# Performance work log

Measured on AMD Instinct MI355X. Metric: run time of the kernel, lower is better.

Reference implementation:

```python
import jax, jax.numpy as jnp
import numpy as np

B, T, DIM, H = 2, 2048, 1024, 16
HD = DIM // H


def setup_inputs() -> dict:
    key = jax.random.key(0)
    k1, k2, k3 = jax.random.split(key, 3)
    std = 1.0 / np.sqrt(DIM)
    x = jax.random.normal(k1, (B, T, DIM), dtype=jnp.float32)
    # torch Linear(dim, 3*dim).weight is [3*dim, dim]; we store the transposed
    # [dim, 3*dim] layout so forward is x @ W_qkv (same math).
    W_qkv = jax.random.uniform(k2, (DIM, 3 * DIM), dtype=jnp.float32, minval=-std, maxval=std)
    W_proj = jax.random.uniform(k3, (DIM, DIM), dtype=jnp.float32, minval=-std, maxval=std)
    return {"x": x, "W_qkv": W_qkv, "W_proj": W_proj}


def reference(x, W_qkv, W_proj):
    Bv, Tv, C = x.shape
    # qkv projection -> [B, T, 3, H, HD] -> q,k,v each [B, H, T, HD]
    qkv = (x @ W_qkv).reshape(Bv, Tv, 3, H, HD)
    qkv = jnp.transpose(qkv, (2, 0, 3, 1, 4))
    q, k, v = qkv[0], qkv[1], qkv[2]
    scale = jnp.asarray(np.sqrt(HD), dtype=x.dtype)
    scores = jnp.einsum('bhqd,bhkd->bhqk', q, k) / scale
    causal = jnp.tril(jnp.ones((Tv, Tv), dtype=bool))  # [T, T]
    scores = jnp.where(causal[None, None, :, :], scores, -jnp.inf)
    attn = jax.nn.softmax(scores, axis=-1)  # [B, H, T, T]
    # entropy per query position, averaged over heads -> [B, T]
    entropy = -(attn * jnp.log(attn + 1e-9)).sum(axis=-1).mean(axis=1)
    # dropout is identity in eval mode
    out = jnp.einsum('bhqk,bhkd->bhqd', attn, v)
    out = jnp.transpose(out, (0, 2, 1, 3)).reshape(Bv, Tv, C)
    return out @ W_proj, entropy
```

## Files before the change

### kernel.cpp

```cpp
#include <hip/hip_runtime.h>


typedef unsigned short u16;
typedef __attribute__((ext_vector_type(8))) __bf16 bf16x8;
typedef __attribute__((ext_vector_type(4))) float float4v;

#define BQ 2
#define TQ 2048
#define DIMQ 1024
#define HQ 16
#define HDQ 64

__device__ __forceinline__ float4v mfma16(bf16x8 a, bf16x8 b, float4v c) {
    return __builtin_amdgcn_mfma_f32_16x16x32_bf16(a, b, c, 0, 0, 0);
}

__device__ __forceinline__ u16 f2bf(float f) {
    unsigned x = __float_as_uint(f);
    return (u16)((x + 0x7FFFu + ((x >> 16) & 1u)) >> 16);
}

__device__ __forceinline__ uint4 cvt8(float4 a, float4 b) {
    union { uint4 v; u16 u[8]; } r;
    r.u[0] = f2bf(a.x); r.u[1] = f2bf(a.y); r.u[2] = f2bf(a.z); r.u[3] = f2bf(a.w);
    r.u[4] = f2bf(b.x); r.u[5] = f2bf(b.y); r.u[6] = f2bf(b.z); r.u[7] = f2bf(b.w);
    return r.v;
}

__device__ __forceinline__ void async16(const u16* g, u16* l) {
    __builtin_amdgcn_global_load_lds(
        (const __attribute__((address_space(1))) void*)g,
        (__attribute__((address_space(3))) void*)l, 16, 0, 0);
}

__device__ __forceinline__ void tr_tile(
    const float* __restrict__ in, u16* __restrict__ out, int R, int C,
    int tx, int ty, int tid, float (*T)[68])
{
    const int k0 = ty * 64, n0 = tx * 64;
    {
        int r = tid >> 2, cc = (tid & 3) << 4;
        const float* src = in + (size_t)(k0 + r) * C + n0 + cc;
        float4 v0 = ((const float4*)src)[0];
        float4 v1 = ((const float4*)src)[1];
        float4 v2 = ((const float4*)src)[2];
        float4 v3 = ((const float4*)src)[3];
        *(float4*)&T[r][cc + 0]  = v0;
        *(float4*)&T[r][cc + 4]  = v1;
        *(float4*)&T[r][cc + 8]  = v2;
        *(float4*)&T[r][cc + 12] = v3;
    }
    __syncthreads();
    {
        int nr = tid >> 2, kc = (tid & 3) << 4;
        union { uint4 v; u16 u[8]; } o0, o1;
#pragma unroll
        for (int j = 0; j < 8; ++j) o0.u[j] = f2bf(T[kc + j][nr]);
#pragma unroll
        for (int j = 0; j < 8; ++j) o1.u[j] = f2bf(T[kc + 8 + j][nr]);
        u16* dst = out + (size_t)(n0 + nr) * R + k0 + kc;
        ((uint4*)dst)[0] = o0.v;
        *(uint4*)(dst + 8) = o1.v;
    }
}

__global__ __launch_bounds__(256) void prep_kernel(
    const float* __restrict__ x, const float* __restrict__ Wq,
    const float* __restrict__ Wp,
    u16* __restrict__ xb, u16* __restrict__ Wt, u16* __restrict__ Wpt)
{
    __shared__ float T[64][68];
    const int bx = blockIdx.x, tid = threadIdx.x;
    if (bx < 2048) {
        int i = (bx * 256 + tid) * 8;
        float4 a = *(const float4*)(x + i);
        float4 b = *(const float4*)(x + i + 4);
        *(uint4*)(xb + i) = cvt8(a, b);
    } else if (bx < 2816) {
        int bb = bx - 2048;
        tr_tile(Wq, Wt, DIMQ, 3 * DIMQ, bb % 48, bb / 48, tid, T);
    } else {
        int bb = bx - 2816;
        tr_tile(Wp, Wpt, DIMQ, DIMQ, bb & 15, bb >> 4, tid, T);
    }
}

__global__ __launch_bounds__(256) void tr_cvt(
    const float* __restrict__ in, u16* __restrict__ out, int R, int C)
{
    __shared__ float T[64][68];
    tr_tile(in, out, R, C, blockIdx.x, blockIdx.y, threadIdx.x, T);
}

template <int TILEM, int MODE>
__global__ __launch_bounds__(256) void gemm_db(
    const u16* __restrict__ A, const u16* __restrict__ Bt,
    int M, int N, int K,
    u16* __restrict__ Qo, u16* __restrict__ Ko, u16* __restrict__ Vt,
    float* __restrict__ Of, const float* __restrict__ EntIn)
{
    constexpr int MT = TILEM / 32;
    constexpr int AR = TILEM / 64;
    __shared__ u16 As[2][TILEM * 32];
    __shared__ u16 Bs[2][128 * 32];

    const int tid = threadIdx.x;
    const int bm = blockIdx.y, bn = blockIdx.x;
    const int wave = tid >> 6, lane = tid & 63;
    const int quad = lane >> 4, c = lane & 15;
    const int wm = wave >> 1, wn = wave & 1;
    const int x3 = c & 3;

    const float4v z = {0.f, 0.f, 0.f, 0.f};
    float4v acc[MT][4];
#pragma unroll
    for (int mt = 0; mt < MT; ++mt)
#pragma unroll
        for (int tn = 0; tn < 4; ++tn) acc[mt][tn] = z;

    const int srow = tid >> 2;
    const int schunk8 = (((tid & 3) ^ (srow & 3)) << 3);
    const u16* ga = A  + (size_t)(bm * TILEM + srow) * K + schunk8;
    const u16* gb = Bt + (size_t)(bn * 128  + srow) * K + schunk8;

#pragma unroll
    for (int p = 0; p < AR; ++p)
        async16(ga + (size_t)(p * 64) * K, As[0] + p * 2048 + tid * 8);
#pragma unroll
    for (int p = 0; p < 2; ++p)
        async16(gb + (size_t)(p * 64) * K, Bs[0] + p * 2048 + tid * 8);

    const int niter = K >> 5;
    for (int it = 0; it < niter; ++it) {
        __syncthreads();
        if (it + 1 < niter) {
            const int nb = (it + 1) & 1;
            const int kc = (it + 1) * 32;
#pragma unroll
            for (int p = 0; p < AR; ++p)
                async16(ga + kc + (size_t)(p * 64) * K, As[nb] + p * 2048 + tid * 8);
#pragma unroll
            for (int p = 0; p < 2; ++p)
                async16(gb + kc + (size_t)(p * 64) * K, Bs[nb] + p * 2048 + tid * 8);
        }
        const u16* as = As[it & 1];
        const u16* bs = Bs[it & 1];

        bf16x8 af[MT], bfr[4];
#pragma unroll
        for (int mt = 0; mt < MT; ++mt)
            af[mt] = *(const bf16x8*)&as[(wm * (TILEM / 2) + mt * 16 + c) * 32 +
                                         ((quad ^ x3) << 3)];
#pragma unroll
        for (int tn = 0; tn < 4; ++tn)
            bfr[tn] = *(const bf16x8*)&bs[(wn * 64 + tn * 16 + c) * 32 +
                                          ((quad ^ x3) << 3)];
#pragma unroll
        for (int mt = 0; mt < MT; ++mt)
#pragma unroll
            for (int tn = 0; tn < 4; ++tn)
                acc[mt][tn] = mfma16(af[mt], bfr[tn], acc[mt][tn]);
    }

#pragma unroll
    for (int mt = 0; mt < MT; ++mt)
#pragma unroll
        for (int tn = 0; tn < 4; ++tn) {
            int gm0 = bm * TILEM + wm * (TILEM / 2) + mt * 16 + quad * 4;
            int gn  = bn * 128 + wn * 64 + tn * 16 + c;
            if (MODE == 0) {
                int s = gn >> 10, h = (gn >> 6) & 15, d = gn & 63;
                int b = gm0 >> 11, t0 = gm0 & 2047;
                size_t bh = (size_t)(b * HQ + h);
                if (s == 2) {
                    union { unsigned long long w; u16 u[4]; } pk;
#pragma unroll
                    for (int r = 0; r < 4; ++r) pk.u[r] = f2bf(acc[mt][tn][r]);
                    *(unsigned long long*)&Vt[(bh * HDQ + d) * TQ + t0] = pk.w;
                } else {
                    u16* dst = (s == 0) ? Qo : Ko;
                    float sc = (s == 0) ? 0.125f : 1.0f;
#pragma unroll
                    for (int r = 0; r < 4; ++r)
                        dst[(bh * TQ + t0 + r) * HDQ + d] = f2bf(acc[mt][tn][r] * sc);
                }
            } else {
#pragma unroll
                for (int r = 0; r < 4; ++r)
                    Of[(size_t)(gm0 + r) * N + gn] = acc[mt][tn][r];
            }
        }

    if (MODE == 1 && bn == 0 && bm < 16) {
        int i = bm * 256 + tid;
        int b = i >> 11, t = i & 2047;
        float s = 0.f;
#pragma unroll
        for (int h = 0; h < HQ; ++h) s += EntIn[((size_t)(b * HQ + h)) * TQ + t];
        Of[(size_t)BQ * TQ * DIMQ + i] = s * (1.0f / HQ);
    }
}

__global__ __launch_bounds__(256) void attn_kernel(
    const u16* __restrict__ Q, const u16* __restrict__ K,
    const u16* __restrict__ Vt, u16* __restrict__ AO,
    float* __restrict__ Ent)
{
    const int qt1 = blockIdx.x;
    const int qt2 = 31 - qt1;
    const int bh = blockIdx.y;
    const int tid = threadIdx.x;
    const int wave = tid >> 6, lane = tid & 63;
    const int quad = lane >> 4, c = lane & 15;
    const int x7 = c & 7;

    __shared__ u16 Ks[2][64 * 64];
    __shared__ u16 Vs[2][64 * 64];
    __shared__ u16 Ps[4][16 * 64];

    const u16* Qp = Q  + (size_t)bh * TQ * HDQ;
    const u16* Kp = K  + (size_t)bh * TQ * HDQ;
    const u16* Vp = Vt + (size_t)bh * HDQ * TQ;

    const int q0[2] = { qt1 * 64 + wave * 16, qt2 * 64 + wave * 16 };

    bf16x8 qf[2][2];
#pragma unroll
    for (int s = 0; s < 2; ++s) {
        const u16* qr = Qp + (size_t)(q0[s] + c) * HDQ;
        qf[s][0] = *(const bf16x8*)(qr + quad * 8);
        qf[s][1] = *(const bf16x8*)(qr + 32 + quad * 8);
    }

    const float4v z = {0.f, 0.f, 0.f, 0.f};
    float4v oacc[2][4];
#pragma unroll
    for (int s = 0; s < 2; ++s)
#pragma unroll
        for (int tn = 0; tn < 4; ++tn) oacc[s][tn] = z;
    float lp[2] = {0.f, 0.f}, tp[2] = {0.f, 0.f};
    const float MX = 12.0f;

    u16* psw = &Ps[wave][0];
    const int ntile = qt2 + 1;

    const int srow = tid >> 3;
    const int schunk8 = (((tid & 7) ^ (srow & 7)) << 3);
    const u16* ka = Kp + (size_t)srow * HDQ + schunk8;
    const u16* va = Vp + (size_t)srow * TQ + schunk8;

    {
        async16(ka, Ks[0] + tid * 8);
        async16(ka + (size_t)32 * HDQ, Ks[0] + 2048 + tid * 8);
        async16(va, Vs[0] + tid * 8);
        async16(va + (size_t)32 * TQ, Vs[0] + 2048 + tid * 8);
    }

    for (int jt = 0; jt < ntile; ++jt) {
        __syncthreads();
        if (jt + 1 < ntile) {
            int nb = (jt + 1) & 1;
            async16(ka + (size_t)((jt + 1) * 64) * HDQ, Ks[nb] + tid * 8);
            async16(ka + (size_t)((jt + 1) * 64 + 32) * HDQ, Ks[nb] + 2048 + tid * 8);
            async16(va + (jt + 1) * 64, Vs[nb] + tid * 8);
            async16(va + (size_t)32 * TQ + (jt + 1) * 64, Vs[nb] + 2048 + tid * 8);
        }
        const u16* ksb = Ks[jt & 1];
        const u16* vsb = Vs[jt & 1];

        bf16x8 kf[4][2], vf[4][2];
#pragma unroll
        for (int tn = 0; tn < 4; ++tn) {
            int base = (tn * 16 + c) * 64;
            kf[tn][0] = *(const bf16x8*)&ksb[base + ((quad ^ x7) << 3)];
            kf[tn][1] = *(const bf16x8*)&ksb[base + (((quad + 4) ^ x7) << 3)];
            vf[tn][0] = *(const bf16x8*)&vsb[base + ((quad ^ x7) << 3)];
            vf[tn][1] = *(const bf16x8*)&vsb[base + (((quad + 4) ^ x7) << 3)];
        }

#pragma unroll
        for (int s = 0; s < 2; ++s) {
            if (s == 0 && jt > qt1) continue;
            const int diag = s ? qt2 : qt1;
#pragma unroll
            for (int tn = 0; tn < 4; ++tn) {
                float4v sacc = z;
                sacc = mfma16(kf[tn][0], qf[s][0], sacc);
                sacc = mfma16(kf[tn][1], qf[s][1], sacc);
                if (jt == diag) {
#pragma unroll
                    for (int r = 0; r < 4; ++r) {
                        int kg = jt * 64 + tn * 16 + quad * 4 + r;
                        if (kg > q0[s] + c) sacc[r] = -1e30f;
                    }
                }
                unsigned u[4];
#pragma unroll
                for (int r = 0; r < 4; ++r) {
                    float sv = sacc[r];
                    float p = __expf(sv - MX);
                    lp[s] += p;
                    tp[s] += p * sv;
                    u[r] = __float_as_uint(p);
                }
                uint2 pk;
                pk.x = (u[0] >> 16) | (u[1] & 0xffff0000u);
                pk.y = (u[2] >> 16) | (u[3] & 0xffff0000u);
                int kc8 = tn * 2 + (quad >> 1);
                *(uint2*)&psw[c * 64 + ((kc8 ^ x7) << 3) + (quad & 1) * 4] = pk;
            }
            bf16x8 pf0 = *(const bf16x8*)&psw[c * 64 + ((quad ^ x7) << 3)];
            bf16x8 pf1 = *(const bf16x8*)&psw[c * 64 + (((quad + 4) ^ x7) << 3)];
#pragma unroll
            for (int tn = 0; tn < 4; ++tn) {
                oacc[s][tn] = mfma16(vf[tn][0], pf0, oacc[s][tn]);
                oacc[s][tn] = mfma16(vf[tn][1], pf1, oacc[s][tn]);
            }
        }
    }

#pragma unroll
    for (int s = 0; s < 2; ++s) {
        lp[s] += __shfl_xor(lp[s], 16); lp[s] += __shfl_xor(lp[s], 32);
        tp[s] += __shfl_xor(tp[s], 16); tp[s] += __shfl_xor(tp[s], 32);
    }

    const int b = bh >> 4, h = bh & 15;
#pragma unroll
    for (int s = 0; s < 2; ++s) {
        float inv = 1.0f / lp[s];
        u16* dst = AO + ((size_t)(b * TQ + q0[s] + c)) * DIMQ + h * HDQ;
#pragma unroll
        for (int tn = 0; tn < 4; ++tn) {
            unsigned u[4];
#pragma unroll
            for (int r = 0; r < 4; ++r)
                u[r] = (unsigned)f2bf(oacc[s][tn][r] * inv);
            uint2 pk;
            pk.x = u[0] | (u[1] << 16);
            pk.y = u[2] | (u[3] << 16);
            *(uint2*)(dst + tn * 16 + quad * 4) = pk;
        }
        if (quad == 0)
            Ent[(size_t)bh * TQ + q0[s] + c] =
                MX + logf(lp[s]) - tp[s] / lp[s];
    }
}

extern "C" void kernel_launch(void* const* d_in, const int* in_sizes, int n_in,
                              void* d_out, int out_size, void* d_ws, size_t ws_size,
                              hipStream_t stream) {
    const float* x     = (const float*)d_in[0];
    const float* Wqkv  = (const float*)d_in[1];
    const float* Wproj = (const float*)d_in[2];
    float* out = (float*)d_out;

    const size_t NE = (size_t)BQ * HQ * TQ * HDQ;
    const size_t WQN = (size_t)3 * DIMQ * DIMQ;
    const size_t WPN = (size_t)DIMQ * DIMQ;
    u16* Qb  = (u16*)d_ws;
    u16* Kb  = Qb + NE;
    u16* Vtb = Kb + NE;
    u16* xb  = Vtb + NE;
    u16* Wt  = xb + NE;
    u16* AO  = xb;

    const size_t need = (4 * NE + WQN + WPN) * 2 + (size_t)BQ * HQ * TQ * 4;
    const bool room = ws_size >= need;
    u16* Wpt = room ? (Wt + WQN) : Wt;
    float* Ent = room ? (float*)(Wpt + WPN) : (float*)(Wt + WQN);

    prep_kernel<<<dim3(room ? 3072 : 2816), 256, 0, stream>>>(
        x, Wqkv, Wproj, xb, Wt, Wpt);
    gemm_db<128, 0><<<dim3(24, 32), 256, 0, stream>>>(
        xb, Wt, BQ * TQ, 3 * DIMQ, DIMQ, Qb, Kb, Vtb, nullptr, nullptr);
    if (!room)
        tr_cvt<<<dim3(16, 16), 256, 0, stream>>>(Wproj, Wpt, DIMQ, DIMQ);
    attn_kernel<<<dim3(16, BQ * HQ), 256, 0, stream>>>(Qb, Kb, Vtb, AO, Ent);
    gemm_db<64, 1><<<dim3(8, 64), 256, 0, stream>>>(
        AO, Wpt, BQ * TQ, DIMQ, DIMQ, nullptr, nullptr, nullptr, out, Ent);
}
```

Before: 177.1 us.

## Triple-buffer GEMM and attention LDS tiles with explicit vmcnt waits

Both the GEMM and attention kernels move from double- to triple-buffered async global-to-LDS loads, prefetching two stages ahead. The __syncthreads at the top of each iteration becomes an inline-asm s_waitcnt vmcnt(N)+s_barrier, so only the oldest stage's loads are awaited. The aim is to hide more memory latency. In exchange the kernels use more LDS, which may reduce occupancy, and correctness now depends on the hand-counted vmcnt values and on the compiler emitting no other outstanding vector memory ops.

```diff
diff --git a/kernel.cpp b/kernel.cpp
--- a/kernel.cpp
+++ b/kernel.cpp
@@ -32,6 +32,8 @@
         (const __attribute__((address_space(1))) void*)g,
         (__attribute__((address_space(3))) void*)l, 16, 0, 0);
 }
+
+#define WAIT_BAR(N) asm volatile("s_waitcnt vmcnt(" #N ")\n\ts_barrier" ::: "memory")
 
 __device__ __forceinline__ void tr_tile(
     const float* __restrict__ in, u16* __restrict__ out, int R, int C,
@@ -101,8 +103,8 @@
 {
     constexpr int MT = TILEM / 32;
     constexpr int AR = TILEM / 64;
-    __shared__ u16 As[2][TILEM * 32];
-    __shared__ u16 Bs[2][128 * 32];
+    __shared__ u16 As[3 * TILEM * 32];
+    __shared__ u16 Bs[3 * 128 * 32];
 
     const int tid = threadIdx.x;
     const int bm = blockIdx.y, bn = blockIdx.x;
@@ -123,28 +125,34 @@
     const u16* ga = A  + (size_t)(bm * TILEM + srow) * K + schunk8;
     const u16* gb = Bt + (size_t)(bn * 128  + srow) * K + schunk8;
 
-#pragma unroll
-    for (int p = 0; p < AR; ++p)
-        async16(ga + (size_t)(p * 64) * K, As[0] + p * 2048 + tid * 8);
-#pragma unroll
-    for (int p = 0; p < 2; ++p)
-        async16(gb + (size_t)(p * 64) * K, Bs[0] + p * 2048 + tid * 8);
+    auto stage = [&](int it) {
+        const int bi = it % 3;
+        u16* as = As + bi * (TILEM * 32);
+        u16* bs = Bs + bi * (128 * 32);
+        const int kc = it * 32;
+#pragma unroll
+        for (int p = 0; p < AR; ++p)
+            async16(ga + kc + (size_t)(p * 64) * K, as + p * 2048 + tid * 8);
+#pragma unroll
+        for (int p = 0; p < 2; ++p)
+            async16(gb + kc + (size_t)(p * 64) * K, bs + p * 2048 + tid * 8);
+    };
 
     const int niter = K >> 5;
+    stage(0);
+    stage(1);
+
     for (int it = 0; it < niter; ++it) {
-        __syncthreads();
         if (it + 1 < niter) {
-            const int nb = (it + 1) & 1;
-            const int kc = (it + 1) * 32;
-#pragma unroll
-            for (int p = 0; p < AR; ++p)
-                async16(ga + kc + (size_t)(p * 64) * K, As[nb] + p * 2048 + tid * 8);
-#pragma unroll
-            for (int p = 0; p < 2; ++p)
-                async16(gb + kc + (size_t)(p * 64) * K, Bs[nb] + p * 2048 + tid * 8);
-        }
-        const u16* as = As[it & 1];
-        const u16* bs = Bs[it & 1];
+            if constexpr (TILEM == 128) WAIT_BAR(4);
+            else                        WAIT_BAR(3);
+        } else {
+            WAIT_BAR(0);
+        }
+        if (it + 2 < niter) stage(it + 2);
+
+        const u16* as = As + (it % 3) * (TILEM * 32);
+        const u16* bs = Bs + (it % 3) * (128 * 32);
 
         bf16x8 af[MT], bfr[4];
 #pragma unroll
@@ -214,8 +222,8 @@
     const int quad = lane >> 4, c = lane & 15;
     const int x7 = c & 7;
 
-    __shared__ u16 Ks[2][64 * 64];
-    __shared__ u16 Vs[2][64 * 64];
+    __shared__ u16 Ks[3 * 4096];
+    __shared__ u16 Vs[3 * 4096];
     __shared__ u16 Ps[4][16 * 64];
 
     const u16* Qp = Q  + (size_t)bh * TQ * HDQ;
@@ -249,24 +257,26 @@
     const u16* ka = Kp + (size_t)srow * HDQ + schunk8;
     const u16* va = Vp + (size_t)srow * TQ + schunk8;
 
-    {
-        async16(ka, Ks[0] + tid * 8);
-        async16(ka + (size_t)32 * HDQ, Ks[0] + 2048 + tid * 8);
-        async16(va, Vs[0] + tid * 8);
-        async16(va + (size_t)32 * TQ, Vs[0] + 2048 + tid * 8);
-    }
+    auto stage = [&](int j) {
+        const int bi = j % 3;
+        u16* kb = Ks + bi * 4096;
+        u16* vb = Vs + bi * 4096;
+        async16(ka + (size_t)(j * 64) * HDQ, kb + tid * 8);
+        async16(ka + (size_t)(j * 64 + 32) * HDQ, kb + 2048 + tid * 8);
+        async16(va + j * 64, vb + tid * 8);
+        async16(va + (size_t)32 * TQ + j * 64, vb + 2048 + tid * 8);
+    };
+
+    stage(0);
+    stage(1);
 
     for (int jt = 0; jt < ntile; ++jt) {
-        __syncthreads();
-        if (jt + 1 < ntile) {
-            int nb = (jt + 1) & 1;
-            async16(ka + (size_t)((jt + 1) * 64) * HDQ, Ks[nb] + tid * 8);
-            async16(ka + (size_t)((jt + 1) * 64 + 32) * HDQ, Ks[nb] + 2048 + tid * 8);
-            async16(va + (jt + 1) * 64, Vs[nb] + tid * 8);
-            async16(va + (size_t)32 * TQ + (jt + 1) * 64, Vs[nb] + 2048 + tid * 8);
-        }
-        const u16* ksb = Ks[jt & 1];
-        const u16* vsb = Vs[jt & 1];
+        if (jt + 1 < ntile) WAIT_BAR(4);
+        else                WAIT_BAR(0);
+        if (jt + 2 < ntile) stage(jt + 2);
+
+        const u16* ksb = Ks + (jt % 3) * 4096;
+        const u16* vsb = Vs + (jt % 3) * 4096;
 
         bf16x8 kf[4][2], vf[4][2];
 #pragma unroll
```

Measured after the change: 180.3 us. About the same (+1.8%).

## Split paired query tiles across separate waves with 512-thread attention blocks

Applied to the files above, without the earlier changes.

The attention kernel now runs 8 waves per block. Waves 0-3 handle the first query tile of the causal pair and waves 4-7 handle the mirrored tile, where before each wave processed both tiles in sequence. Each thread now issues one K and one V async load per stage, and per-wave accumulator state is halved. This raises parallelism and cuts register pressure. The cost is idle waves once the shorter tile finishes, since they still wait at every block barrier, plus larger blocks that limit scheduling flexibility.

```diff
diff --git a/kernel.cpp b/kernel.cpp
--- a/kernel.cpp
+++ b/kernel.cpp
@@ -201,7 +201,7 @@
     }
 }
 
-__global__ __launch_bounds__(256) void attn_kernel(
+__global__ __launch_bounds__(512, 4) void attn_kernel(
     const u16* __restrict__ Q, const u16* __restrict__ K,
     const u16* __restrict__ Vt, u16* __restrict__ AO,
     float* __restrict__ Ent)
@@ -210,88 +210,74 @@
     const int qt2 = 31 - qt1;
     const int bh = blockIdx.y;
     const int tid = threadIdx.x;
-    const int wave = tid >> 6, lane = tid & 63;
+    const int wave = tid >> 6;
+    const int lane = tid & 63;
     const int quad = lane >> 4, c = lane & 15;
     const int x7 = c & 7;
 
-    __shared__ u16 Ks[2][64 * 64];
-    __shared__ u16 Vs[2][64 * 64];
-    __shared__ u16 Ps[4][16 * 64];
+    __shared__ u16 Ks[2][4096];
+    __shared__ u16 Vs[2][4096];
+    __shared__ u16 Ps[8][1024];
 
     const u16* Qp = Q  + (size_t)bh * TQ * HDQ;
     const u16* Kp = K  + (size_t)bh * TQ * HDQ;
     const u16* Vp = Vt + (size_t)bh * HDQ * TQ;
 
-    const int q0[2] = { qt1 * 64 + wave * 16, qt2 * 64 + wave * 16 };
-
-    bf16x8 qf[2][2];
-#pragma unroll
-    for (int s = 0; s < 2; ++s) {
-        const u16* qr = Qp + (size_t)(q0[s] + c) * HDQ;
-        qf[s][0] = *(const bf16x8*)(qr + quad * 8);
-        qf[s][1] = *(const bf16x8*)(qr + 32 + quad * 8);
-    }
+    const int mytile = (wave < 4) ? qt1 : qt2;
+    const int q0 = mytile * 64 + (wave & 3) * 16;
+
+    const u16* qr = Qp + (size_t)(q0 + c) * HDQ;
+    bf16x8 qf0 = *(const bf16x8*)(qr + quad * 8);
+    bf16x8 qf1 = *(const bf16x8*)(qr + 32 + quad * 8);
 
     const float4v z = {0.f, 0.f, 0.f, 0.f};
-    float4v oacc[2][4];
-#pragma unroll
-    for (int s = 0; s < 2; ++s)
-#pragma unroll
-        for (int tn = 0; tn < 4; ++tn) oacc[s][tn] = z;
-    float lp[2] = {0.f, 0.f}, tp[2] = {0.f, 0.f};
+    float4v oacc[4] = {z, z, z, z};
+    float lp = 0.f, tp = 0.f;
     const float MX = 12.0f;
 
     u16* psw = &Ps[wave][0];
     const int ntile = qt2 + 1;
 
     const int srow = tid >> 3;
-    const int schunk8 = (((tid & 7) ^ (srow & 7)) << 3);
-    const u16* ka = Kp + (size_t)srow * HDQ + schunk8;
-    const u16* va = Vp + (size_t)srow * TQ + schunk8;
-
-    {
-        async16(ka, Ks[0] + tid * 8);
-        async16(ka + (size_t)32 * HDQ, Ks[0] + 2048 + tid * 8);
-        async16(va, Vs[0] + tid * 8);
-        async16(va + (size_t)32 * TQ, Vs[0] + 2048 + tid * 8);
-    }
+    const int sch = ((tid & 7) ^ (srow & 7)) << 3;
+    const u16* ka = Kp + (size_t)srow * HDQ + sch;
+    const u16* va = Vp + (size_t)srow * TQ + sch;
+
+    async16(ka, Ks[0] + tid * 8);
+    async16(va, Vs[0] + tid * 8);
 
     for (int jt = 0; jt < ntile; ++jt) {
         __syncthreads();
         if (jt + 1 < ntile) {
             int nb = (jt + 1) & 1;
             async16(ka + (size_t)((jt + 1) * 64) * HDQ, Ks[nb] + tid * 8);
-            async16(ka + (size_t)((jt + 1) * 64 + 32) * HDQ, Ks[nb] + 2048 + tid * 8);
             async16(va + (jt + 1) * 64, Vs[nb] + tid * 8);
-            async16(va + (size_t)32 * TQ + (jt + 1) * 64, Vs[nb] + 2048 + tid * 8);
-        }
-        const u16* ksb = Ks[jt & 1];
-        const u16* vsb = Vs[jt & 1];
-
-        bf16x8 kf[4][2], vf[4][2];
-#pragma unroll
-        for (int tn = 0; tn < 4; ++tn) {
-            int base = (tn * 16 + c) * 64;
-            kf[tn][0] = *(const bf16x8*)&ksb[base + ((quad ^ x7) << 3)];
-            kf[tn][1] = *(const bf16x8*)&ksb[base + (((quad + 4) ^ x7) << 3)];
-            vf[tn][0] = *(const bf16x8*)&vsb[base + ((quad ^ x7) << 3)];
-            vf[tn][1] = *(const bf16x8*)&vsb[base + (((quad + 4) ^ x7) << 3)];
-        }
-
-#pragma unroll
-        for (int s = 0; s < 2; ++s) {
-            if (s == 0 && jt > qt1) continue;
-            const int diag = s ? qt2 : qt1;
+        }
+
+        if (jt <= mytile) {
+            const u16* ksb = Ks[jt & 1];
+            const u16* vsb = Vs[jt & 1];
+
+            bf16x8 kf[4][2], vf[4][2];
+#pragma unroll
+            for (int tn = 0; tn < 4; ++tn) {
+                int base = (tn * 16 + c) * 64;
+                kf[tn][0] = *(const bf16x8*)&ksb[base + ((quad ^ x7) << 3)];
+                kf[tn][1] = *(const bf16x8*)&ksb[base + (((quad + 4) ^ x7) << 3)];
+                vf[tn][0] = *(const bf16x8*)&vsb[base + ((quad ^ x7) << 3)];
+                vf[tn][1] = *(const bf16x8*)&vsb[base + (((quad + 4) ^ x7) << 3)];
+            }
+
 #pragma unroll
             for (int tn = 0; tn < 4; ++tn) {
                 float4v sacc = z;
-                sacc = mfma16(kf[tn][0], qf[s][0], sacc);
-                sacc = mfma16(kf[tn][1], qf[s][1], sacc);
-                if (jt == diag) {
+                sacc = mfma16(kf[tn][0], qf0, sacc);
+                sacc = mfma16(kf[tn][1], qf1, sacc);
+                if (jt == mytile) {
 #pragma unroll
                     for (int r = 0; r < 4; ++r) {
                         int kg = jt * 64 + tn * 16 + quad * 4 + r;
-                        if (kg > q0[s] + c) sacc[r] = -1e30f;
+                        if (kg > q0 + c) sacc[r] = -1e30f;
                     }
                 }
                 unsigned u[4];
@@ -299,8 +285,8 @@
                 for (int r = 0; r < 4; ++r) {
                     float sv = sacc[r];
                     float p = __expf(sv - MX);
-                    lp[s] += p;
-                    tp[s] += p * sv;
+                    lp += p;
+                    tp += p * sv;
                     u[r] = __float_as_uint(p);
                 }
                 uint2 pk;
@@ -313,37 +299,32 @@
             bf16x8 pf1 = *(const bf16x8*)&psw[c * 64 + (((quad + 4) ^ x7) << 3)];
 #pragma unroll
             for (int tn = 0; tn < 4; ++tn) {
-                oacc[s][tn] = mfma16(vf[tn][0], pf0, oacc[s][tn]);
-                oacc[s][tn] = mfma16(vf[tn][1], pf1, oacc[s][tn]);
+                oacc[tn] = mfma16(vf[tn][0], pf0, oacc[tn]);
+                oacc[tn] = mfma16(vf[tn][1], pf1, oacc[tn]);
             }
         }
     }
 
-#pragma unroll
-    for (int s = 0; s < 2; ++s) {
-        lp[s] += __shfl_xor(lp[s], 16); lp[s] += __shfl_xor(lp[s], 32);
-        tp[s] += __shfl_xor(tp[s], 16); tp[s] += __shfl_xor(tp[s], 32);
-    }
+    lp += __shfl_xor(lp, 16); lp += __shfl_xor(lp, 32);
+    tp += __shfl_xor(tp, 16); tp += __shfl_xor(tp, 32);
 
     const int b = bh >> 4, h = bh & 15;
-#pragma unroll
-    for (int s = 0; s < 2; ++s) {
-        float inv = 1.0f / lp[s];
-        u16* dst = AO + ((size_t)(b * TQ + q0[s] + c)) * DIMQ + h * HDQ;
+    {
+        float inv = 1.0f / lp;
+        u16* dst = AO + ((size_t)(b * TQ + q0 + c)) * DIMQ + h * HDQ;
 #pragma unroll
         for (int tn = 0; tn < 4; ++tn) {
             unsigned u[4];
 #pragma unroll
             for (int r = 0; r < 4; ++r)
-                u[r] = (unsigned)f2bf(oacc[s][tn][r] * inv);
+                u[r] = (unsigned)f2bf(oacc[tn][r] * inv);
             uint2 pk;
             pk.x = u[0] | (u[1] << 16);
             pk.y = u[2] | (u[3] << 16);
             *(uint2*)(dst + tn * 16 + quad * 4) = pk;
         }
         if (quad == 0)
-            Ent[(size_t)bh * TQ + q0[s] + c] =
-                MX + logf(lp[s]) - tp[s] / lp[s];
+            Ent[(size_t)bh * TQ + q0 + c] = MX + logf(lp) - tp / lp;
     }
 }
 
@@ -376,7 +357,7 @@
         xb, Wt, BQ * TQ, 3 * DIMQ, DIMQ, Qb, Kb, Vtb, nullptr, nullptr);
     if (!room)
         tr_cvt<<<dim3(16, 16), 256, 0, stream>>>(Wproj, Wpt, DIMQ, DIMQ);
-    attn_kernel<<<dim3(16, BQ * HQ), 256, 0, stream>>>(Qb, Kb, Vtb, AO, Ent);
+    attn_kernel<<<dim3(16, BQ * HQ), 512, 0, stream>>>(Qb, Kb, Vtb, AO, Ent);
     gemm_db<64, 1><<<dim3(8, 64), 256, 0, stream>>>(
         AO, Wpt, BQ * TQ, DIMQ, DIMQ, nullptr, nullptr, nullptr, out, Ent);
 }
```

Result: no change. 177.4 us (+0.1%).
